# Optimization experiments

Hardware: AMD Instinct MI355X
Metric: run time of the kernel (lower is better)

Reference implementation:

```python
import jax, jax.numpy as jnp
import numpy as np

NEAR, FAR, N_SAMPLES = 1.0, 6.0, 64
FAR_APPEND = 1000.0


def setup_inputs() -> dict:
    key = jax.random.key(0)
    ks = jax.random.split(key, 8)
    B, R = 2, 4096
    # pixel coords in a 128x128 image
    x_pix = jax.random.uniform(ks[0], (B, R, 2), dtype=jnp.float32) * 128.0
    # plausible pinhole intrinsics (fx=fy=128, cx=cy=64)
    K = jnp.array([[128.0, 0.0, 64.0], [0.0, 128.0, 64.0], [0.0, 0.0, 1.0]], dtype=jnp.float32)
    intrinsics = jnp.tile(K[None], (B, 1, 1))
    # identity rotation, small translation cam2world
    c2w = jnp.eye(4, dtype=jnp.float32).at[:3, 3].set(jnp.array([0.1, -0.2, 0.5]))
    cam2world = jnp.tile(c2w[None], (B, 1, 1))
    H = 256
    W1 = jax.random.normal(ks[1], (3, H), dtype=jnp.float32) / np.sqrt(3.0)
    b1 = jnp.zeros((H,), jnp.float32)
    W2 = jax.random.normal(ks[2], (H, H), dtype=jnp.float32) / np.sqrt(H)
    b2 = jnp.zeros((H,), jnp.float32)
    W3 = jax.random.normal(ks[3], (H, 4), dtype=jnp.float32) / np.sqrt(H)
    b3 = jnp.zeros((4,), jnp.float32)
    return {"x_pix": x_pix, "intrinsics": intrinsics, "cam2world": cam2world,
            "W1": W1, "b1": b1, "W2": W2, "b2": b2, "W3": W3, "b3": b3}


def _radiance_field(pts, W1, b1, W2, b2, W3, b3):
    # pts: (B, N, 3) -> sigma (B, N, 1), rad (B, N, 3)
    h = jax.nn.relu(pts @ W1 + b1)
    h = jax.nn.relu(h @ W2 + b2)
    o = h @ W3 + b3
    return jax.nn.relu(o[..., :1]), jax.nn.sigmoid(o[..., 1:])


def _get_world_rays(x_pix, intrinsics, cam2world):
    B, R, _ = x_pix.shape
    inv_K = jnp.linalg.inv(intrinsics)  # (B,3,3)
    xy_hom = jnp.concatenate([x_pix, jnp.ones((B, R, 1), x_pix.dtype)], axis=-1)  # (B,R,3)
    dirs_cam = jnp.einsum("bij,brj->bri", inv_K, xy_hom)  # unnormalized cam-frame dirs
    dirs_hom = jnp.concatenate([dirs_cam, jnp.zeros((B, R, 1), x_pix.dtype)], axis=-1)  # w=0 vector
    dirs_world = jnp.einsum("bij,brj->bri", cam2world, dirs_hom)[..., :3]
    origins = jnp.broadcast_to(cam2world[:, None, :3, 3], (B, R, 3))
    return origins, dirs_world


def _volume_integral(z_vals, sigmas, radiances):
    # z_vals: (S,); sigmas: (B,R,S,1); radiances: (B,R,S,3)
    dists = jnp.diff(z_vals, append=jnp.array([FAR_APPEND], z_vals.dtype))  # (S,)
    alpha = 1.0 - jnp.exp(-sigmas * dists[None, None, :, None])  # (B,R,S,1)
    Ts = jnp.cumprod(1.0 - alpha, axis=2)  # inclusive cumprod, matching torch
    weights = alpha * Ts  # (B,R,S,1)
    rgb = jnp.sum(weights * radiances, axis=2)  # (B,R,3)
    depth_map = jnp.einsum("brsv,s->brv", weights, z_vals)  # (B,R,1)
    return rgb, depth_map, weights


def reference(x_pix, intrinsics, cam2world, W1, b1, W2, b2, W3, b3):
    B, R = x_pix.shape[0], x_pix.shape[1]
    ros, rds = _get_world_rays(x_pix, intrinsics, cam2world)
    z_vals = jnp.linspace(NEAR, FAR, N_SAMPLES, dtype=x_pix.dtype)  # (S,)
    pts = ros[:, :, None, :] + rds[:, :, None, :] * z_vals[None, None, :, None]  # (B,R,S,3)
    pts = pts.reshape(B, -1, 3)
    sigma, rad = _radiance_field(pts, W1, b1, W2, b2, W3, b3)
    sigma = sigma.reshape(B, R, N_SAMPLES, 1)
    rad = rad.reshape(B, R, N_SAMPLES, 3)
    rgb, depth_map, weights = _volume_integral(z_vals, sigma, rad)
    accum = jnp.sum(weights, axis=-2)  # (B,R,1)
    rgb = rgb + (1.0 - accum)  # white background
    return rgb, depth_map
```

## Files before the change

kernel.cpp:

```cpp
#include <hip/hip_runtime.h>

typedef unsigned short u16;
typedef _Float16 f16x8 __attribute__((ext_vector_type(8)));
typedef float    f32x4  __attribute__((ext_vector_type(4)));
typedef float    f32x16 __attribute__((ext_vector_type(16)));

#define NRAYS 8192

#define WS_W2T  0
#define WS_B2   131072
#define WS_W3   132096
#define WS_B3   136192
#define WS_W1   136208
#define WS_B1   139280
#define WS_INTR 140304
#define WS_C2W  140384

__device__ __forceinline__ float bf2f(u16 u){
  union { unsigned int i; float f; } v; v.i = ((unsigned int)u) << 16; return v.f;
}
__device__ __forceinline__ u16 f2h(float f){
  union { _Float16 h; u16 u; } v; v.h = (_Float16)f;
  return v.u;
}
__device__ __forceinline__ int detect_bf16(const void* intr){
  return (((const u16*)intr)[0] == 0x4300u) ? 1 : 0;
}

__device__ __forceinline__ void conv_arr(const void* src, float* dst, int n, int bf, int tid){
  if (bf){
    const u16* s = (const u16*)src;
    for (int i = tid; i < n; i += 256) dst[i] = bf2f(s[i]);
  } else {
    const float* s = (const float*)src;
    for (int i = tid; i < n; i += 256) dst[i] = s[i];
  }
}

__global__ void prep(const void* __restrict__ W2, const void* __restrict__ W1,
                     const void* __restrict__ b1, const void* __restrict__ b2,
                     const void* __restrict__ W3, const void* __restrict__ b3,
                     const void* __restrict__ intr, const void* __restrict__ c2w,
                     char* __restrict__ ws)
{
  const int bf = detect_bf16(intr);
  const int t = threadIdx.x;
  if (blockIdx.x == 16){
    conv_arr(W1,  (float*)(ws + WS_W1),  768,  bf, t);
    conv_arr(b1,  (float*)(ws + WS_B1),  256,  bf, t);
    conv_arr(b2,  (float*)(ws + WS_B2),  256,  bf, t);
    conv_arr(W3,  (float*)(ws + WS_W3),  1024, bf, t);
    conv_arr(b3,  (float*)(ws + WS_B3),  4,    bf, t);
    conv_arr(intr,(float*)(ws + WS_INTR),18,   bf, t);
    conv_arr(c2w, (float*)(ws + WS_C2W), 32,   bf, t);
    return;
  }
  __shared__ u16 tile[64][72];
  const int bx = blockIdx.x & 3;
  const int by = blockIdx.x >> 2;
  const int c = t & 63, rb = t >> 6;
  u16* W2T = (u16*)(ws + WS_W2T);
  #pragma unroll
  for (int rr = 0; rr < 64; rr += 4){
    int k = bx*64 + rr + rb;
    int n = by*64 + c;
    float v = bf ? bf2f(((const u16*)W2)[k*256 + n]) : ((const float*)W2)[k*256 + n];
    tile[rr + rb][c] = f2h(v);
  }
  __syncthreads();
  #pragma unroll
  for (int rr = 0; rr < 64; rr += 4){
    int n = by*64 + rr + rb;
    int k = bx*64 + c;
    W2T[n*256 + k] = tile[c][rr + rb];
  }
}

__global__ __launch_bounds__(256, 2) void nerf_fused(
    const void* __restrict__ x_pix,
    const void* __restrict__ intr,
    const char* __restrict__ ws,
    float* __restrict__ out)
{
  __shared__ __align__(16) u16   h1s[128 * 256];
  __shared__ __align__(16) float obuf[4 * 128 * 4];
  __shared__ __align__(16) float cbuf[1280];

  const int tid = threadIdx.x;
  const int l   = tid & 63;
  const int w   = tid >> 6;
  const int ray = w >> 1;
  const int rayg = blockIdx.x * 2 + ray;
  const int bb   = rayg >> 12;
  const int bf   = detect_bf16(intr);

  const float* intrf = (const float*)(ws + WS_INTR);
  const float* c2wf  = (const float*)(ws + WS_C2W);
  const float* W1f   = (const float*)(ws + WS_W1);
  const float* b1f   = (const float*)(ws + WS_B1);
  const float* b2f   = (const float*)(ws + WS_B2);
  const float* W3f   = (const float*)(ws + WS_W3);
  const u16*   W2T   = (const u16*)(ws + WS_W2T);

  float stg0 = b2f[tid];
  float stg1 = W3f[tid];
  float stg2 = W3f[tid + 256];
  float stg3 = W3f[tid + 512];
  float stg4 = W3f[tid + 768];

  float px, py;
  if (bf){
    px = bf2f(((const u16*)x_pix)[rayg*2 + 0]);
    py = bf2f(((const u16*)x_pix)[rayg*2 + 1]);
  } else {
    px = ((const float*)x_pix)[rayg*2 + 0];
    py = ((const float*)x_pix)[rayg*2 + 1];
  }
  float Ka[9], Mm[16];
  #pragma unroll
  for (int i = 0; i < 9;  i++) Ka[i] = intrf[bb*9  + i];
  #pragma unroll
  for (int i = 0; i < 16; i++) Mm[i] = c2wf[bb*16 + i];
  float a = Ka[0], b_ = Ka[1], c = Ka[2];
  float d = Ka[3], e  = Ka[4], f = Ka[5];
  float g = Ka[6], h_ = Ka[7], i9 = Ka[8];
  float det = a*(e*i9 - f*h_) - b_*(d*i9 - f*g) + c*(d*h_ - e*g);
  float inv = 1.0f / det;
  float i00 = (e*i9 - f*h_)*inv, i01 = (c*h_ - b_*i9)*inv, i02 = (b_*f - c*e)*inv;
  float i10 = (f*g - d*i9)*inv, i11 = (a*i9 - c*g)*inv, i12 = (c*d - a*f)*inv;
  float i20 = (d*h_ - e*g)*inv, i21 = (b_*g - a*h_)*inv, i22 = (a*e - b_*d)*inv;
  float dcx = i00*px + i01*py + i02;
  float dcy = i10*px + i11*py + i12;
  float dcz = i20*px + i21*py + i22;
  float dx = Mm[0]*dcx + Mm[1]*dcy + Mm[2]*dcz;
  float dy = Mm[4]*dcx + Mm[5]*dcy + Mm[6]*dcz;
  float dz = Mm[8]*dcx + Mm[9]*dcy + Mm[10]*dcz;
  float ox = Mm[3], oy = Mm[7], oz = Mm[11];

  const int kbase = (w & 1)*128 + l*2;
  float aa0, aa1, gg0, gg1;
  {
    float2 r0 = *(const float2*)(W1f + kbase);
    float2 r1 = *(const float2*)(W1f + 256 + kbase);
    float2 r2 = *(const float2*)(W1f + 512 + kbase);
    float2 rb = *(const float2*)(b1f + kbase);
    aa0 = ox*r0.x + oy*r1.x + oz*r2.x + rb.x;
    aa1 = ox*r0.y + oy*r1.y + oz*r2.y + rb.y;
    gg0 = dx*r0.x + dy*r1.x + dz*r2.x;
    gg1 = dx*r0.y + dy*r1.y + dz*r2.y;
  }
  const float step = 5.0f / 63.0f;
  const int chunk_w = ((w & 1) << 4) + (l >> 2);
  const int sub_b   = (l & 3) << 2;
  {
    char* hb = (char*)h1s + (ray*64)*512;
    #pragma unroll 8
    for (int s = 0; s < 64; s++){
      float z = 1.0f + step * (float)s;
      u16 e0 = f2h(fmaxf(fmaf(gg0, z, aa0), 0.0f));
      u16 e1 = f2h(fmaxf(fmaf(gg1, z, aa1), 0.0f));
      unsigned pk = (unsigned)e0 | ((unsigned)e1 << 16);
      *(unsigned*)(hb + s*512 + ((chunk_w ^ (s & 7)) << 4) + sub_b) = pk;
    }
  }

  cbuf[tid]        = stg0;
  cbuf[256 + tid]  = stg1;
  cbuf[512 + tid]  = stg2;
  cbuf[768 + tid]  = stg3;
  cbuf[1024 + tid] = stg4;
  __syncthreads();

  const int l31 = l & 31;
  const int h   = l >> 5;
  const int m7  = l31 & 7;
  const int nbase = w * 64;

  f32x16 acc[2][4];
  #pragma unroll
  for (int nt = 0; nt < 2; nt++)
    #pragma unroll
    for (int mt = 0; mt < 4; mt++)
      acc[nt][mt] = (f32x16){0.f,0.f,0.f,0.f,0.f,0.f,0.f,0.f,
                             0.f,0.f,0.f,0.f,0.f,0.f,0.f,0.f};

  const u16* Arow = W2T + (nbase + l31)*256 + h*8;
  const char* hbase = (const char*)h1s;

  f16x8 ap[3][2];
  #pragma unroll
  for (int pp = 0; pp < 3; pp++){
    ap[pp][0] = *(const f16x8*)(Arow + pp*16);
    ap[pp][1] = *(const f16x8*)(Arow + 32*256 + pp*16);
  }
  f16x8 bcur[4];
  {
    const int swz0 = ((0 + h) ^ m7) << 4;
    #pragma unroll
    for (int mt = 0; mt < 4; mt++)
      bcur[mt] = *(const f16x8*)(hbase + (mt*32 + l31)*512 + swz0);
  }

  #pragma unroll
  for (int t = 0; t < 16; t++){
    const int sl = t % 3;
    f16x8 a0 = ap[sl][0];
    f16x8 a1 = ap[sl][1];
    if (t + 3 < 16){
      ap[sl][0] = *(const f16x8*)(Arow + (t+3)*16);
      ap[sl][1] = *(const f16x8*)(Arow + 32*256 + (t+3)*16);
    }
    f16x8 bnxt[4];
    if (t < 15){
      const int swzn = ((2*(t+1) + h) ^ m7) << 4;
      #pragma unroll
      for (int mt = 0; mt < 4; mt++)
        bnxt[mt] = *(const f16x8*)(hbase + (mt*32 + l31)*512 + swzn);
    }
    #pragma unroll
    for (int nt = 0; nt < 2; nt++)
      #pragma unroll
      for (int mt = 0; mt < 4; mt++)
        acc[nt][mt] = __builtin_amdgcn_mfma_f32_32x32x16_f16(
            nt == 0 ? a0 : a1, bcur[mt], acc[nt][mt], 0, 0, 0);
    if (t < 15){
      #pragma unroll
      for (int mt = 0; mt < 4; mt++) bcur[mt] = bnxt[mt];
    }
  }

  f32x4 o_m[4];
  #pragma unroll
  for (int mt = 0; mt < 4; mt++) o_m[mt] = (f32x4){0.f,0.f,0.f,0.f};

  #pragma unroll
  for (int nt = 0; nt < 2; nt++){
    #pragma unroll
    for (int gq = 0; gq < 4; gq++){
      const int n0 = nbase + nt*32 + gq*8 + h*4;
      f32x4 b2v = *(const f32x4*)(cbuf + n0);
      f32x4 w30 = *(const f32x4*)(cbuf + 256 + n0*4);
      f32x4 w31 = *(const f32x4*)(cbuf + 256 + (n0+1)*4);
      f32x4 w32 = *(const f32x4*)(cbuf + 256 + (n0+2)*4);
      f32x4 w33 = *(const f32x4*)(cbuf + 256 + (n0+3)*4);
      #pragma unroll
      for (int mt = 0; mt < 4; mt++){
        float h0 = fmaxf(acc[nt][mt][gq*4+0] + b2v.x, 0.0f);
        float h1 = fmaxf(acc[nt][mt][gq*4+1] + b2v.y, 0.0f);
        float h2 = fmaxf(acc[nt][mt][gq*4+2] + b2v.z, 0.0f);
        float h3 = fmaxf(acc[nt][mt][gq*4+3] + b2v.w, 0.0f);
        o_m[mt] = o_m[mt] + h0*w30 + h1*w31 + h2*w32 + h3*w33;
      }
    }
  }

  #pragma unroll
  for (int mt = 0; mt < 4; mt++)
    #pragma unroll
    for (int j = 0; j < 4; j++){
      float v = o_m[mt][j];
      v += __shfl_xor(v, 32, 64);
      o_m[mt][j] = v;
    }

  if (h == 0){
    #pragma unroll
    for (int mt = 0; mt < 4; mt++)
      *(f32x4*)&obuf[(w*128 + mt*32 + l31)*4] = o_m[mt];
  }
  __syncthreads();

  if (w < 2){
    const int m = w*64 + l;
    const f32x4* ob4 = (const f32x4*)obuf;
    f32x4 oj  = ob4[m] + ob4[128 + m] + ob4[256 + m] + ob4[384 + m];
    f32x4 b3v = *(const f32x4*)(ws + WS_B3);
    float o_s0 = oj.x + b3v.x;
    float o_s1 = oj.y + b3v.y;
    float o_s2 = oj.z + b3v.z;
    float o_s3 = oj.w + b3v.w;

    const float zc    = 1.0f + step * (float)l;
    const float znext = (l == 63) ? 1000.0f : (1.0f + step * (float)(l + 1));
    const float dist  = znext - zc;
    float sigma = fmaxf(o_s0, 0.0f);
    float alpha = 1.0f - __expf(-sigma * dist);
    float t = 1.0f - alpha;
    #pragma unroll
    for (int sh = 1; sh < 64; sh <<= 1){
      float u = __shfl_up(t, sh, 64);
      if (l >= sh) t *= u;
    }
    float wgt = alpha * t;
    float r0 = 1.0f / (1.0f + __expf(-o_s1));
    float r1 = 1.0f / (1.0f + __expf(-o_s2));
    float r2 = 1.0f / (1.0f + __expf(-o_s3));
    float s0 = wgt*r0, s1 = wgt*r1, s2 = wgt*r2, sw = wgt, sz = wgt*zc;
    #pragma unroll
    for (int sh = 1; sh < 64; sh <<= 1){
      s0 += __shfl_xor(s0, sh, 64);
      s1 += __shfl_xor(s1, sh, 64);
      s2 += __shfl_xor(s2, sh, 64);
      sw += __shfl_xor(sw, sh, 64);
      sz += __shfl_xor(sz, sh, 64);
    }
    if (l == 0){
      const int rg = blockIdx.x*2 + w;
      float bg = 1.0f - sw;
      out[rg*3 + 0] = s0 + bg;
      out[rg*3 + 1] = s1 + bg;
      out[rg*3 + 2] = s2 + bg;
      out[3*NRAYS + rg] = sz;
    }
  }
}

extern "C" void kernel_launch(void* const* d_in, const int* in_sizes, int n_in,
                              void* d_out, int out_size, void* d_ws, size_t ws_size,
                              hipStream_t stream)
{
  const void* x_pix = d_in[0];
  const void* intr  = d_in[1];
  const void* c2w   = d_in[2];
  const void* W1    = d_in[3];
  const void* b1    = d_in[4];
  const void* W2    = d_in[5];
  const void* b2    = d_in[6];
  const void* W3    = d_in[7];
  const void* b3    = d_in[8];
  float* outp = (float*)d_out;
  char*  ws   = (char*)d_ws;

  hipLaunchKernelGGL(prep, dim3(17), dim3(256), 0, stream,
                     W2, W1, b1, b2, W3, b3, intr, c2w, ws);
  hipLaunchKernelGGL(nerf_fused, dim3(NRAYS/2), dim3(256), 0, stream,
                     x_pix, intr, ws, outp);
}
```

Before: 165.9 us.

## Make nerf kernel persistent over 8 ray pairs with overlapped tail

Each block now processes 8 pairs of rays in a loop instead of one, with the grid shrunk by 8x. Per-block setup (constant staging into LDS, matrix inverse, origin-dependent layer-1 terms) is amortized across iterations. The next pixel coordinate is prefetched, and the volume-integral tail of the previous iteration runs on two waves while the next hidden layer is being written, overlapping scalar work with the MFMA phase. The cost is fewer blocks, 512, which may underfill the GPU, plus W2 fragments reloaded every iteration.

```diff
diff --git a/kernel.cpp b/kernel.cpp
--- a/kernel.cpp
+++ b/kernel.cpp
@@ -90,9 +90,8 @@
   const int l   = tid & 63;
   const int w   = tid >> 6;
   const int ray = w >> 1;
-  const int rayg = blockIdx.x * 2 + ray;
-  const int bb   = rayg >> 12;
-  const int bf   = detect_bf16(intr);
+  const int bf  = detect_bf16(intr);
+  const int bb  = (int)(blockIdx.x >> 8);
 
   const float* intrf = (const float*)(ws + WS_INTR);
   const float* c2wf  = (const float*)(ws + WS_C2W);
@@ -102,20 +101,12 @@
   const float* W3f   = (const float*)(ws + WS_W3);
   const u16*   W2T   = (const u16*)(ws + WS_W2T);
 
-  float stg0 = b2f[tid];
-  float stg1 = W3f[tid];
-  float stg2 = W3f[tid + 256];
-  float stg3 = W3f[tid + 512];
-  float stg4 = W3f[tid + 768];
-
-  float px, py;
-  if (bf){
-    px = bf2f(((const u16*)x_pix)[rayg*2 + 0]);
-    py = bf2f(((const u16*)x_pix)[rayg*2 + 1]);
-  } else {
-    px = ((const float*)x_pix)[rayg*2 + 0];
-    py = ((const float*)x_pix)[rayg*2 + 1];
-  }
+  cbuf[tid]        = b2f[tid];
+  cbuf[256 + tid]  = W3f[tid];
+  cbuf[512 + tid]  = W3f[tid + 256];
+  cbuf[768 + tid]  = W3f[tid + 512];
+  cbuf[1024 + tid] = W3f[tid + 768];
+
   float Ka[9], Mm[16];
   #pragma unroll
   for (int i = 0; i < 9;  i++) Ka[i] = intrf[bb*9  + i];
@@ -129,190 +120,215 @@
   float i00 = (e*i9 - f*h_)*inv, i01 = (c*h_ - b_*i9)*inv, i02 = (b_*f - c*e)*inv;
   float i10 = (f*g - d*i9)*inv, i11 = (a*i9 - c*g)*inv, i12 = (c*d - a*f)*inv;
   float i20 = (d*h_ - e*g)*inv, i21 = (b_*g - a*h_)*inv, i22 = (a*e - b_*d)*inv;
-  float dcx = i00*px + i01*py + i02;
-  float dcy = i10*px + i11*py + i12;
-  float dcz = i20*px + i21*py + i22;
-  float dx = Mm[0]*dcx + Mm[1]*dcy + Mm[2]*dcz;
-  float dy = Mm[4]*dcx + Mm[5]*dcy + Mm[6]*dcz;
-  float dz = Mm[8]*dcx + Mm[9]*dcy + Mm[10]*dcz;
   float ox = Mm[3], oy = Mm[7], oz = Mm[11];
 
   const int kbase = (w & 1)*128 + l*2;
-  float aa0, aa1, gg0, gg1;
-  {
-    float2 r0 = *(const float2*)(W1f + kbase);
-    float2 r1 = *(const float2*)(W1f + 256 + kbase);
-    float2 r2 = *(const float2*)(W1f + 512 + kbase);
-    float2 rb = *(const float2*)(b1f + kbase);
-    aa0 = ox*r0.x + oy*r1.x + oz*r2.x + rb.x;
-    aa1 = ox*r0.y + oy*r1.y + oz*r2.y + rb.y;
-    gg0 = dx*r0.x + dy*r1.x + dz*r2.x;
-    gg1 = dx*r0.y + dy*r1.y + dz*r2.y;
-  }
+  const float2 r0 = *(const float2*)(W1f + kbase);
+  const float2 r1 = *(const float2*)(W1f + 256 + kbase);
+  const float2 r2 = *(const float2*)(W1f + 512 + kbase);
+  const float2 rbv = *(const float2*)(b1f + kbase);
+  const float aaB0 = ox*r0.x + oy*r1.x + oz*r2.x + rbv.x;
+  const float aaB1 = ox*r0.y + oy*r1.y + oz*r2.y + rbv.y;
+
+  const f32x4 b3v = *(const f32x4*)(ws + WS_B3);
+
   const float step = 5.0f / 63.0f;
   const int chunk_w = ((w & 1) << 4) + (l >> 2);
   const int sub_b   = (l & 3) << 2;
-  {
-    char* hb = (char*)h1s + (ray*64)*512;
-    #pragma unroll 8
-    for (int s = 0; s < 64; s++){
-      float z = 1.0f + step * (float)s;
-      u16 e0 = f2h(fmaxf(fmaf(gg0, z, aa0), 0.0f));
-      u16 e1 = f2h(fmaxf(fmaf(gg1, z, aa1), 0.0f));
-      unsigned pk = (unsigned)e0 | ((unsigned)e1 << 16);
-      *(unsigned*)(hb + s*512 + ((chunk_w ^ (s & 7)) << 4) + sub_b) = pk;
-    }
-  }
-
-  cbuf[tid]        = stg0;
-  cbuf[256 + tid]  = stg1;
-  cbuf[512 + tid]  = stg2;
-  cbuf[768 + tid]  = stg3;
-  cbuf[1024 + tid] = stg4;
-  __syncthreads();
 
   const int l31 = l & 31;
   const int h   = l >> 5;
   const int m7  = l31 & 7;
   const int nbase = w * 64;
-
-  f32x16 acc[2][4];
-  #pragma unroll
-  for (int nt = 0; nt < 2; nt++)
-    #pragma unroll
-    for (int mt = 0; mt < 4; mt++)
-      acc[nt][mt] = (f32x16){0.f,0.f,0.f,0.f,0.f,0.f,0.f,0.f,
-                             0.f,0.f,0.f,0.f,0.f,0.f,0.f,0.f};
-
   const u16* Arow = W2T + (nbase + l31)*256 + h*8;
   const char* hbase = (const char*)h1s;
 
-  f16x8 ap[3][2];
-  #pragma unroll
-  for (int pp = 0; pp < 3; pp++){
-    ap[pp][0] = *(const f16x8*)(Arow + pp*16);
-    ap[pp][1] = *(const f16x8*)(Arow + 32*256 + pp*16);
-  }
-  f16x8 bcur[4];
-  {
-    const int swz0 = ((0 + h) ^ m7) << 4;
+  auto loadpx = [&](int itq, float& qx, float& qy){
+    const int rg = (blockIdx.x*8 + itq)*2 + ray;
+    if (bf){
+      qx = bf2f(((const u16*)x_pix)[rg*2 + 0]);
+      qy = bf2f(((const u16*)x_pix)[rg*2 + 1]);
+    } else {
+      qx = ((const float*)x_pix)[rg*2 + 0];
+      qy = ((const float*)x_pix)[rg*2 + 1];
+    }
+  };
+
+  auto do_tail = [&](int itp){
+    if ((w >> 1) == (itp & 1)){
+      const int r = w & 1;
+      const int m = r*64 + l;
+      const f32x4* ob4 = (const f32x4*)obuf;
+      f32x4 oj  = ob4[m] + ob4[128 + m] + ob4[256 + m] + ob4[384 + m];
+      float o_s0 = oj.x + b3v.x;
+      float o_s1 = oj.y + b3v.y;
+      float o_s2 = oj.z + b3v.z;
+      float o_s3 = oj.w + b3v.w;
+
+      const float zc    = 1.0f + step * (float)l;
+      const float znext = (l == 63) ? 1000.0f : (1.0f + step * (float)(l + 1));
+      const float dist  = znext - zc;
+      float sigma = fmaxf(o_s0, 0.0f);
+      float alpha = 1.0f - __expf(-sigma * dist);
+      float t = 1.0f - alpha;
+      #pragma unroll
+      for (int sh = 1; sh < 64; sh <<= 1){
+        float u = __shfl_up(t, sh, 64);
+        if (l >= sh) t *= u;
+      }
+      float wgt = alpha * t;
+      float q0 = 1.0f / (1.0f + __expf(-o_s1));
+      float q1 = 1.0f / (1.0f + __expf(-o_s2));
+      float q2 = 1.0f / (1.0f + __expf(-o_s3));
+      float s0 = wgt*q0, s1 = wgt*q1, s2 = wgt*q2, sw = wgt, sz = wgt*zc;
+      #pragma unroll
+      for (int sh = 1; sh < 64; sh <<= 1){
+        s0 += __shfl_xor(s0, sh, 64);
+        s1 += __shfl_xor(s1, sh, 64);
+        s2 += __shfl_xor(s2, sh, 64);
+        sw += __shfl_xor(sw, sh, 64);
+        sz += __shfl_xor(sz, sh, 64);
+      }
+      if (l == 0){
+        const int rg = (blockIdx.x*8 + itp)*2 + r;
+        float bg = 1.0f - sw;
+        out[rg*3 + 0] = s0 + bg;
+        out[rg*3 + 1] = s1 + bg;
+        out[rg*3 + 2] = s2 + bg;
+        out[3*NRAYS + rg] = sz;
+      }
+    }
+  };
+
+  float pxc, pyc;
+  loadpx(0, pxc, pyc);
+
+  for (int it = 0; it < 8; ++it){
+    float pxn = 0.0f, pyn = 0.0f;
+    if (it < 7) loadpx(it + 1, pxn, pyn);
+
+    float dcx = i00*pxc + i01*pyc + i02;
+    float dcy = i10*pxc + i11*pyc + i12;
+    float dcz = i20*pxc + i21*pyc + i22;
+    float dx = Mm[0]*dcx + Mm[1]*dcy + Mm[2]*dcz;
+    float dy = Mm[4]*dcx + Mm[5]*dcy + Mm[6]*dcz;
+    float dz = Mm[8]*dcx + Mm[9]*dcy + Mm[10]*dcz;
+    float aa0 = aaB0, aa1 = aaB1;
+    float gg0 = dx*r0.x + dy*r1.x + dz*r2.x;
+    float gg1 = dx*r0.y + dy*r1.y + dz*r2.y;
+
+    f16x8 ap[3][2];
+    #pragma unroll
+    for (int pp = 0; pp < 3; pp++){
+      ap[pp][0] = *(const f16x8*)(Arow + pp*16);
+      ap[pp][1] = *(const f16x8*)(Arow + 32*256 + pp*16);
+    }
+
+    {
+      char* hb = (char*)h1s + (ray*64)*512;
+      #pragma unroll 8
+      for (int s = 0; s < 64; s++){
+        float z = 1.0f + step * (float)s;
+        u16 e0 = f2h(fmaxf(fmaf(gg0, z, aa0), 0.0f));
+        u16 e1 = f2h(fmaxf(fmaf(gg1, z, aa1), 0.0f));
+        unsigned pk = (unsigned)e0 | ((unsigned)e1 << 16);
+        *(unsigned*)(hb + s*512 + ((chunk_w ^ (s & 7)) << 4) + sub_b) = pk;
+      }
+    }
+
+    if (it > 0) do_tail(it - 1);
+
+    __syncthreads();
+
+    f32x16 acc[2][4];
+    #pragma unroll
+    for (int nt = 0; nt < 2; nt++)
+      #pragma unroll
+      for (int mt = 0; mt < 4; mt++)
+        acc[nt][mt] = (f32x16){0.f,0.f,0.f,0.f,0.f,0.f,0.f,0.f,
+                               0.f,0.f,0.f,0.f,0.f,0.f,0.f,0.f};
+
+    f16x8 bcur[4];
+    {
+      const int swz0 = ((0 + h) ^ m7) << 4;
+      #pragma unroll
+      for (int mt = 0; mt < 4; mt++)
+        bcur[mt] = *(const f16x8*)(hbase + (mt*32 + l31)*512 + swz0);
+    }
+
+    #pragma unroll
+    for (int t = 0; t < 16; t++){
+      const int sl = t % 3;
+      f16x8 a0 = ap[sl][0];
+      f16x8 a1 = ap[sl][1];
+      if (t + 3 < 16){
+        ap[sl][0] = *(const f16x8*)(Arow + (t+3)*16);
+        ap[sl][1] = *(const f16x8*)(Arow + 32*256 + (t+3)*16);
+      }
+      f16x8 bnxt[4];
+      if (t < 15){
+        const int swzn = ((2*(t+1) + h) ^ m7) << 4;
+        #pragma unroll
+        for (int mt = 0; mt < 4; mt++)
+          bnxt[mt] = *(const f16x8*)(hbase + (mt*32 + l31)*512 + swzn);
+      }
+      #pragma unroll
+      for (int nt = 0; nt < 2; nt++)
+        #pragma unroll
+        for (int mt = 0; mt < 4; mt++)
+          acc[nt][mt] = __builtin_amdgcn_mfma_f32_32x32x16_f16(
+              nt == 0 ? a0 : a1, bcur[mt], acc[nt][mt], 0, 0, 0);
+      if (t < 15){
+        #pragma unroll
+        for (int mt = 0; mt < 4; mt++) bcur[mt] = bnxt[mt];
+      }
+    }
+
+    f32x4 o_m[4];
+    #pragma unroll
+    for (int mt = 0; mt < 4; mt++) o_m[mt] = (f32x4){0.f,0.f,0.f,0.f};
+
+    #pragma unroll
+    for (int nt = 0; nt < 2; nt++){
+      #pragma unroll
+      for (int gq = 0; gq < 4; gq++){
+        const int n0 = nbase + nt*32 + gq*8 + h*4;
+        f32x4 b2v = *(const f32x4*)(cbuf + n0);
+        f32x4 w30 = *(const f32x4*)(cbuf + 256 + n0*4);
+        f32x4 w31 = *(const f32x4*)(cbuf + 256 + (n0+1)*4);
+        f32x4 w32 = *(const f32x4*)(cbuf + 256 + (n0+2)*4);
+        f32x4 w33 = *(const f32x4*)(cbuf + 256 + (n0+3)*4);
+        #pragma unroll
+        for (int mt = 0; mt < 4; mt++){
+          float h0 = fmaxf(acc[nt][mt][gq*4+0] + b2v.x, 0.0f);
+          float h1 = fmaxf(acc[nt][mt][gq*4+1] + b2v.y, 0.0f);
+          float h2 = fmaxf(acc[nt][mt][gq*4+2] + b2v.z, 0.0f);
+          float h3 = fmaxf(acc[nt][mt][gq*4+3] + b2v.w, 0.0f);
+          o_m[mt] = o_m[mt] + h0*w30 + h1*w31 + h2*w32 + h3*w33;
+        }
+      }
+    }
+
     #pragma unroll
     for (int mt = 0; mt < 4; mt++)
-      bcur[mt] = *(const f16x8*)(hbase + (mt*32 + l31)*512 + swz0);
-  }
-
-  #pragma unroll
-  for (int t = 0; t < 16; t++){
-    const int sl = t % 3;
-    f16x8 a0 = ap[sl][0];
-    f16x8 a1 = ap[sl][1];
-    if (t + 3 < 16){
-      ap[sl][0] = *(const f16x8*)(Arow + (t+3)*16);
-      ap[sl][1] = *(const f16x8*)(Arow + 32*256 + (t+3)*16);
-    }
-    f16x8 bnxt[4];
-    if (t < 15){
-      const int swzn = ((2*(t+1) + h) ^ m7) << 4;
+      #pragma unroll
+      for (int j = 0; j < 4; j++){
+        float v = o_m[mt][j];
+        v += __shfl_xor(v, 32, 64);
+        o_m[mt][j] = v;
+      }
+
+    if (h == 0){
       #pragma unroll
       for (int mt = 0; mt < 4; mt++)
-        bnxt[mt] = *(const f16x8*)(hbase + (mt*32 + l31)*512 + swzn);
-    }
-    #pragma unroll
-    for (int nt = 0; nt < 2; nt++)
-      #pragma unroll
-      for (int mt = 0; mt < 4; mt++)
-        acc[nt][mt] = __builtin_amdgcn_mfma_f32_32x32x16_f16(
-            nt == 0 ? a0 : a1, bcur[mt], acc[nt][mt], 0, 0, 0);
-    if (t < 15){
-      #pragma unroll
-      for (int mt = 0; mt < 4; mt++) bcur[mt] = bnxt[mt];
-    }
-  }
-
-  f32x4 o_m[4];
-  #pragma unroll
-  for (int mt = 0; mt < 4; mt++) o_m[mt] = (f32x4){0.f,0.f,0.f,0.f};
-
-  #pragma unroll
-  for (int nt = 0; nt < 2; nt++){
-    #pragma unroll
-    for (int gq = 0; gq < 4; gq++){
-      const int n0 = nbase + nt*32 + gq*8 + h*4;
-      f32x4 b2v = *(const f32x4*)(cbuf + n0);
-      f32x4 w30 = *(const f32x4*)(cbuf + 256 + n0*4);
-      f32x4 w31 = *(const f32x4*)(cbuf + 256 + (n0+1)*4);
-      f32x4 w32 = *(const f32x4*)(cbuf + 256 + (n0+2)*4);
-      f32x4 w33 = *(const f32x4*)(cbuf + 256 + (n0+3)*4);
-      #pragma unroll
-      for (int mt = 0; mt < 4; mt++){
-        float h0 = fmaxf(acc[nt][mt][gq*4+0] + b2v.x, 0.0f);
-        float h1 = fmaxf(acc[nt][mt][gq*4+1] + b2v.y, 0.0f);
-        float h2 = fmaxf(acc[nt][mt][gq*4+2] + b2v.z, 0.0f);
-        float h3 = fmaxf(acc[nt][mt][gq*4+3] + b2v.w, 0.0f);
-        o_m[mt] = o_m[mt] + h0*w30 + h1*w31 + h2*w32 + h3*w33;
-      }
-    }
-  }
-
-  #pragma unroll
-  for (int mt = 0; mt < 4; mt++)
-    #pragma unroll
-    for (int j = 0; j < 4; j++){
-      float v = o_m[mt][j];
-      v += __shfl_xor(v, 32, 64);
-      o_m[mt][j] = v;
-    }
-
-  if (h == 0){
-    #pragma unroll
-    for (int mt = 0; mt < 4; mt++)
-      *(f32x4*)&obuf[(w*128 + mt*32 + l31)*4] = o_m[mt];
-  }
-  __syncthreads();
-
-  if (w < 2){
-    const int m = w*64 + l;
-    const f32x4* ob4 = (const f32x4*)obuf;
-    f32x4 oj  = ob4[m] + ob4[128 + m] + ob4[256 + m] + ob4[384 + m];
-    f32x4 b3v = *(const f32x4*)(ws + WS_B3);
-    float o_s0 = oj.x + b3v.x;
-    float o_s1 = oj.y + b3v.y;
-    float o_s2 = oj.z + b3v.z;
-    float o_s3 = oj.w + b3v.w;
-
-    const float zc    = 1.0f + step * (float)l;
-    const float znext = (l == 63) ? 1000.0f : (1.0f + step * (float)(l + 1));
-    const float dist  = znext - zc;
-    float sigma = fmaxf(o_s0, 0.0f);
-    float alpha = 1.0f - __expf(-sigma * dist);
-    float t = 1.0f - alpha;
-    #pragma unroll
-    for (int sh = 1; sh < 64; sh <<= 1){
-      float u = __shfl_up(t, sh, 64);
-      if (l >= sh) t *= u;
-    }
-    float wgt = alpha * t;
-    float r0 = 1.0f / (1.0f + __expf(-o_s1));
-    float r1 = 1.0f / (1.0f + __expf(-o_s2));
-    float r2 = 1.0f / (1.0f + __expf(-o_s3));
-    float s0 = wgt*r0, s1 = wgt*r1, s2 = wgt*r2, sw = wgt, sz = wgt*zc;
-    #pragma unroll
-    for (int sh = 1; sh < 64; sh <<= 1){
-      s0 += __shfl_xor(s0, sh, 64);
-      s1 += __shfl_xor(s1, sh, 64);
-      s2 += __shfl_xor(s2, sh, 64);
-      sw += __shfl_xor(sw, sh, 64);
-      sz += __shfl_xor(sz, sh, 64);
-    }
-    if (l == 0){
-      const int rg = blockIdx.x*2 + w;
-      float bg = 1.0f - sw;
-      out[rg*3 + 0] = s0 + bg;
-      out[rg*3 + 1] = s1 + bg;
-      out[rg*3 + 2] = s2 + bg;
-      out[3*NRAYS + rg] = sz;
-    }
-  }
+        *(f32x4*)&obuf[(w*128 + mt*32 + l31)*4] = o_m[mt];
+    }
+    __syncthreads();
+
+    pxc = pxn; pyc = pyn;
+  }
+
+  do_tail(7);
 }
 
 extern "C" void kernel_launch(void* const* d_in, const int* in_sizes, int n_in,
@@ -333,6 +349,6 @@
 
   hipLaunchKernelGGL(prep, dim3(17), dim3(256), 0, stream,
                      W2, W1, b1, b2, W3, b3, intr, c2w, ws);
-  hipLaunchKernelGGL(nerf_fused, dim3(NRAYS/2), dim3(256), 0, stream,
+  hipLaunchKernelGGL(nerf_fused, dim3(NRAYS/16), dim3(256), 0, stream,
                      x_pix, intr, ws, outp);
 }
```

After: 237.6 us. +43.2%, slower.
